# Optimization experiments

Hardware: AMD Instinct MI355X
Metric: run time of the kernel (lower is better)

Reference implementation:

```python
import jax, jax.numpy as jnp
import numpy as np

BN_EPS = 1e-5

def _l2norm(x, axis):
    # F.normalize: x / max(||x||_2, 1e-12)
    n = jnp.sqrt(jnp.sum(x * x, axis=axis, keepdims=True))
    return x / jnp.maximum(n, 1e-12)

def _psi(x_bhc, w, g, b):
    # 1x1 conv over HW-as-channels: [B,HW,C] x [D,HW] -> [B,D,C]
    y = jnp.einsum('dh,bhc->bdc', w, x_bhc)
    # inference BatchNorm2d with running_mean=0, running_var=1
    scale = g / jnp.sqrt(1.0 + BN_EPS)
    y = y * scale[None, :, None] + b[None, :, None]
    return jax.nn.relu(y)

def setup_inputs() -> dict:
    key = jax.random.key(0)
    ks = jax.random.split(key, 8)
    B, C, H, W, D = 16, 2048, 32, 32, 256
    return {
        'v2l_conv_feature': jax.random.normal(ks[0], (B, C, H, W), jnp.float32),
        'l2v_conv_feature': jax.random.normal(ks[1], (B, C, H, W), jnp.float32),
        'w_v2l': jax.random.normal(ks[2], (D, H * W), jnp.float32) * 0.02,
        'g_v2l': jax.random.uniform(ks[3], (D,), jnp.float32, 0.5, 1.5),
        'b_v2l': jax.random.normal(ks[4], (D,), jnp.float32) * 0.1,
        'w_l2v': jax.random.normal(ks[5], (D, H * W), jnp.float32) * 0.02,
        'g_l2v': jax.random.uniform(ks[6], (D,), jnp.float32, 0.5, 1.5),
        'b_l2v': jax.random.normal(ks[7], (D,), jnp.float32) * 0.1,
    }

def reference(v2l_conv_feature, l2v_conv_feature, w_v2l, g_v2l, b_v2l, w_l2v, g_l2v, b_l2v):
    B, C, H, W = v2l_conv_feature.shape
    HW = H * W
    xv = jnp.transpose(v2l_conv_feature.reshape(B, C, HW), (0, 2, 1))  # [B,HW,C]
    xl = jnp.transpose(l2v_conv_feature.reshape(B, C, HW), (0, 2, 1))  # [B,HW,C]
    v2l_adj = _l2norm(_psi(xv, w_v2l, g_v2l, b_v2l), axis=2)  # [B,D,C], norm over C
    l2v_adj = _l2norm(_psi(xl, w_l2v, g_l2v, b_l2v), axis=1)  # [B,D,C], norm over D
    # Faithful to torch: reshape of the permuted tensor is a raw row-major
    # reinterpretation [B,HW,C] -> [B,C,HW] (NOT a transpose back).
    xv_r = xv.reshape(B, C, HW)
    latent = jnp.einsum('bdc,bch->bdh', v2l_adj, xv_r)          # [B,D,HW]
    latent_n = _l2norm(latent, axis=-1)
    aff = jax.nn.softmax(jnp.einsum('bdh,beh->bde', latent_n, latent_n), axis=-1)  # [B,D,D]
    latent = jnp.einsum('bde,beh->bdh', aff, latent)            # [B,D,HW]
    visible = jnp.einsum('bdc,bdh->bch', l2v_adj, latent)       # [B,C,HW]
    return visible.reshape(B, C, H, W)
```

## Files before the change

kernel.cpp:

```cpp
#include <hip/hip_runtime.h>
#include <hip/hip_bf16.h>

#define BB 16
#define CC 2048
#define HWW 1024
#define DD 256
#define BN_RSQRT 0.9999950000374997f

typedef short bf16x8 __attribute__((ext_vector_type(8)));
typedef float f32x4 __attribute__((ext_vector_type(4)));
typedef unsigned short u16x8 __attribute__((ext_vector_type(8)));
typedef unsigned short u16x4 __attribute__((ext_vector_type(4)));
typedef unsigned short u16;

typedef __attribute__((address_space(1))) const unsigned GU;
typedef __attribute__((address_space(3))) unsigned LU;
__device__ __forceinline__ void gload16(const void* g, void* l) {
    __builtin_amdgcn_global_load_lds((GU*)g, (LU*)l, 16, 0, 0);
}

__device__ __forceinline__ unsigned short f2bf(float x) {
    unsigned u = __builtin_bit_cast(unsigned, x);
    unsigned r = u + 0x7FFFu + ((u >> 16) & 1u);
    return (unsigned short)(r >> 16);
}
__device__ __forceinline__ float bf2f(unsigned short h) {
    unsigned u = ((unsigned)h) << 16;
    return __builtin_bit_cast(float, u);
}
__device__ __forceinline__ void split2(float x, unsigned short& hi, unsigned short& lo) {
    hi = f2bf(x);
    lo = f2bf(x - bf2f(hi));
}
__device__ __forceinline__ void split2t(float x, unsigned short& hi, unsigned short& lo) {
    hi = f2bf(x);
    float d = x - bf2f(hi);
    lo = (unsigned short)(__builtin_bit_cast(unsigned, d) >> 16);
}

struct RegsA { u16x8 h[2]; u16x8 l[2]; };
struct RegsB { u16x8 h[2]; u16x8 l[2]; };

__global__ __launch_bounds__(256) void split_k(const float* __restrict__ in,
                                               u16* __restrict__ hi, u16* __restrict__ lo,
                                               long long n8) {
    long long i = (long long)blockIdx.x * 256 + threadIdx.x;
    if (i >= n8) return;
    const float4* p = (const float4*)in + i * 2;
    float4 a = p[0], b = p[1];
    float xs[8] = {a.x, a.y, a.z, a.w, b.x, b.y, b.z, b.w};
    u16x8 h, l;
    #pragma unroll
    for (int j = 0; j < 8; ++j) { unsigned short hh, ll; split2(xs[j], hh, ll); h[j] = hh; l[j] = ll; }
    *(u16x8*)(hi + i * 8) = h;
    *(u16x8*)(lo + i * 8) = l;
}

template <int BF, int EPI, int FUSE2, int KS>
__global__ __launch_bounds__(512, 4) void gemm2b(
    const u16* __restrict__ Ah0, const u16* __restrict__ Al0,
    const u16* __restrict__ Ah1, const u16* __restrict__ Al1,
    long long aB, int lda,
    const void* __restrict__ B0a, const void* __restrict__ B0b,
    const void* __restrict__ B1a, const void* __restrict__ B1b,
    long long bB, int ldb,
    float* __restrict__ C0, float* __restrict__ C1,
    long long cB, long long kB, int ldc,
    int K,
    const float* __restrict__ g0, const float* __restrict__ bb0,
    const float* __restrict__ g1, const float* __restrict__ bb1)
{
    __shared__ __attribute__((aligned(16))) char smem[2][32768];

    const int gx = gridDim.x, gy = gridDim.y;
    int nwg = gx * gy * gridDim.z;
    int id = blockIdx.x + gx * (blockIdx.y + gy * blockIdx.z);
    int chunk = nwg >> 3;
    int nid = (id & 7) * chunk + (id >> 3);
    int bx = nid % gx;
    int tmp = nid / gx;
    int by = tmp % gy;
    int bz = tmp / gy;

    const int t = threadIdx.x;
    const int n0 = bx * 128, m0 = by * 128;

    int op = 0, batch, kz = 0;
    if constexpr (FUSE2) { op = bz >> 4; batch = bz & 15; }
    else if constexpr (KS > 1) { batch = bz / KS; kz = bz - batch * KS; }
    else { batch = bz; }
    const int koffA = kz * K;

    const u16* Ahp = (op ? Ah1 : Ah0) + (long long)batch * aB + koffA;
    const u16* Alp = (op ? Al1 : Al0) + (long long)batch * aB + koffA;
    const float* Bf = nullptr;
    const u16* Bh = nullptr;
    const u16* Bl = nullptr;
    if constexpr (BF == 0) {
        Bf = (const float*)(op ? B1a : B0a) + (long long)batch * bB;
        Bf += ((long long)(koffA >> 10)) * 1024 * ldb + (koffA & 1023);
    } else {
        Bh = (const u16*)(op ? B1a : B0a) + (long long)batch * bB;
        Bl = (const u16*)(op ? B1b : B0b) + (long long)batch * bB;
    }
    float* Cb = ((EPI == 1 && FUSE2) ? (op ? C1 : C0) : C0)
              + (long long)batch * cB + (long long)kz * kB;
    const float* gp = op ? g1 : g0;
    const float* bp = op ? bb1 : bb0;

    const int arow = t >> 2;
    const int aslt = (t & 3) ^ ((t >> 3) & 3);
    const int brow = t >> 3;
    const int bslt = (t & 7) ^ ((t >> 3) & 7);

    const int l = t & 63, w = t >> 6;
    const int wr = w >> 2, wc = w & 3;
    const int rl = l & 15, kq = l >> 4;
    const int fsw = (kq ^ ((rl >> 1) & 3)) * 16;

    f32x4 acc[4][2];
    #pragma unroll
    for (int i = 0; i < 4; ++i)
        #pragma unroll
        for (int j = 0; j < 2; ++j)
            acc[i][j] = (f32x4){0.f, 0.f, 0.f, 0.f};

    auto gstage = [&](int k0, char* sn) {
        const u16* pa = Ahp + (long long)(m0 + arow) * lda + k0 + aslt * 8;
        gload16(pa, sn + t * 16);
        const u16* pl = Alp + (long long)(m0 + arow) * lda + k0 + aslt * 8;
        gload16(pl, sn + 8192 + t * 16);
        if constexpr (BF == 0) {
            const float* pb = Bf + (long long)(n0 + brow) * ldb + k0 + bslt * 4;
            gload16(pb,                       sn + 16384 + t * 16);
            gload16(pb + (long long)64 * ldb, sn + 24576 + t * 16);
        } else {
            const u16* pbh = Bh + (long long)(n0 + arow) * ldb + k0 + aslt * 8;
            gload16(pbh, sn + 16384 + t * 16);
            const u16* pbl = Bl + (long long)(n0 + arow) * ldb + k0 + aslt * 8;
            gload16(pbl, sn + 24576 + t * 16);
        }
    };

    auto readA = [&](const char* sb, bf16x8* fah, bf16x8* fal) {
        #pragma unroll
        for (int i2 = 0; i2 < 4; ++i2) {
            int off = (wr * 64 + i2 * 16 + rl) * 64 + fsw;
            fah[i2] = *(const bf16x8*)(sb + off);
            fal[i2] = *(const bf16x8*)(sb + 8192 + off);
        }
    };
    auto readB = [&](const char* sb, bf16x8* fbh, bf16x8* fbl) {
        #pragma unroll
        for (int j = 0; j < 2; ++j) {
            int row = wc * 32 + j * 16 + rl;
            if constexpr (BF == 0) {
                const char* p = sb + 16384 + row * 128;
                int g = rl & 7;
                float4 x0 = *(const float4*)(p + ((2 * kq) ^ g) * 16);
                float4 x1 = *(const float4*)(p + ((2 * kq + 1) ^ g) * 16);
                float xs[8] = {x0.x, x0.y, x0.z, x0.w, x1.x, x1.y, x1.z, x1.w};
                u16x8 h, lo;
                #pragma unroll
                for (int e = 0; e < 8; ++e) {
                    unsigned short hh, ll; split2t(xs[e], hh, ll);
                    h[e] = hh; lo[e] = ll;
                }
                fbh[j] = __builtin_bit_cast(bf16x8, h);
                fbl[j] = __builtin_bit_cast(bf16x8, lo);
            } else {
                int off = row * 64 + fsw;
                fbh[j] = *(const bf16x8*)(sb + 16384 + off);
                fbl[j] = *(const bf16x8*)(sb + 24576 + off);
            }
        }
    };

    const int NIT = K >> 5;

    gstage(0, smem[0]);
    asm volatile("s_waitcnt vmcnt(0)" ::: "memory");
    __builtin_amdgcn_s_barrier();

    for (int it = 0; it < NIT; ++it) {
        char* sb = smem[it & 1];
        char* sn = smem[(it + 1) & 1];
        const bool more = (it + 1) < NIT;
        if (more) gstage((it + 1) << 5, sn);

        bf16x8 fah[4], fal[4], fbh[2], fbl[2];
        readB(sb, fbh, fbl);
        readA(sb, fah, fal);

        __builtin_amdgcn_s_setprio(1);
        #pragma unroll
        for (int i2 = 0; i2 < 4; ++i2)
            #pragma unroll
            for (int j = 0; j < 2; ++j)
                acc[i2][j] = __builtin_amdgcn_mfma_f32_16x16x32_bf16(fal[i2], fbh[j], acc[i2][j], 0, 0, 0);
        #pragma unroll
        for (int i2 = 0; i2 < 4; ++i2)
            #pragma unroll
            for (int j = 0; j < 2; ++j)
                acc[i2][j] = __builtin_amdgcn_mfma_f32_16x16x32_bf16(fah[i2], fbl[j], acc[i2][j], 0, 0, 0);
        #pragma unroll
        for (int i2 = 0; i2 < 4; ++i2)
            #pragma unroll
            for (int j = 0; j < 2; ++j)
                acc[i2][j] = __builtin_amdgcn_mfma_f32_16x16x32_bf16(fah[i2], fbh[j], acc[i2][j], 0, 0, 0);
        __builtin_amdgcn_s_setprio(0);

        if (more) { asm volatile("s_waitcnt vmcnt(0)" ::: "memory"); }
        __builtin_amdgcn_s_barrier();
    }

    #pragma unroll
    for (int i = 0; i < 4; ++i) {
        #pragma unroll
        for (int r = 0; r < 4; ++r) {
            int row = m0 + wr * 64 + i * 16 + kq * 4 + r;
            float sc = 1.0f, bi = 0.0f;
            if (EPI == 1) { sc = gp[row] * BN_RSQRT; bi = bp[row]; }
            #pragma unroll
            for (int j = 0; j < 2; ++j) {
                int col = n0 + wc * 32 + j * 16 + rl;
                float v = acc[i][j][r];
                if (EPI == 1) v = fmaxf(fmaf(v, sc, bi), 0.0f);
                Cb[(long long)row * ldc + col] = v;
            }
        }
    }
}

template <int BN_, int EPI>
__global__ __launch_bounds__(256) void mfma_gemm(
    const void* __restrict__ Ap, const void* __restrict__ Ap2, long long aB, int lda,
    const void* __restrict__ Bp, const void* __restrict__ Bp2, long long bB, int ldb,
    void* __restrict__ Cp, void* __restrict__ Cp2,
    long long cB, int ldc, int K)
{
    constexpr int NJ   = BN_ / 32;
    constexpr int BNB  = BN_ * 64;
    constexpr int BUFB = 16384 + BN_ * 128;
    __shared__ __attribute__((aligned(16))) char smem[2][BUFB];

    const int gx = gridDim.x, gy = gridDim.y;
    int nwg = gx * gy * gridDim.z;
    int id = blockIdx.x + gx * (blockIdx.y + gy * blockIdx.z);
    int chunk = nwg >> 3;
    int nid = (id & 7) * chunk + (id >> 3);
    int bx = nid % gx;
    int tmp = nid / gx;
    int by = tmp % gy;
    int bz = tmp / gy;

    const int t  = threadIdx.x;
    const int n0 = bx * BN_;
    const int m0 = by * 128;

    const int ar = t >> 1, ag = t & 1;
    const int af = (ar >> 1) & 3;
    const int as0 = (2 * ag) ^ af, as1 = (2 * ag + 1) ^ af;
    const bool bact = (BN_ == 128) || (t < 2 * BN_);
    const int br = (t >> 1) & (BN_ - 1), bg = t & 1;
    const int bf = (br >> 1) & 3;
    const int bs0 = (2 * bg) ^ bf, bs1 = (2 * bg + 1) ^ bf;

    const int l  = t & 63, w = t >> 6;
    const int wr = w >> 1, wc = w & 1;
    const int rl = l & 15, kq = l >> 4;
    const int sw = kq ^ ((rl >> 1) & 3);
    const int aoff = (wr * 64 + rl) * 64 + sw * 16;
    const int boff = (wc * (BN_ / 2) + rl) * 64 + sw * 16;

    const u16* Ahp = (const u16*)Ap  + (long long)bz * aB;
    const u16* Alp = (const u16*)Ap2 + (long long)bz * aB;
    const u16* Bhp = (const u16*)Bp  + (long long)bz * bB;
    const u16* Blp = (const u16*)Bp2 + (long long)bz * bB;

    auto loadA = [&](int k0, RegsA& ra) {
        const u16* ph = Ahp + (long long)(m0 + ar) * lda + k0 + ag * 16;
        const u16* pl = Alp + (long long)(m0 + ar) * lda + k0 + ag * 16;
        ra.h[0] = *(const u16x8*)(ph);
        ra.h[1] = *(const u16x8*)(ph + 8);
        ra.l[0] = *(const u16x8*)(pl);
        ra.l[1] = *(const u16x8*)(pl + 8);
    };
    auto loadB = [&](int k0, RegsB& rb) {
        if (!bact) return;
        const u16* ph = Bhp + (long long)(n0 + br) * ldb + k0 + bg * 16;
        const u16* pl = Blp + (long long)(n0 + br) * ldb + k0 + bg * 16;
        rb.h[0] = *(const u16x8*)(ph);
        rb.h[1] = *(const u16x8*)(ph + 8);
        rb.l[0] = *(const u16x8*)(pl);
        rb.l[1] = *(const u16x8*)(pl + 8);
    };
    auto stageWrite = [&](char* sb, RegsA& ra, RegsB& rb) {
        *(u16x8*)(sb + ar * 64 + as0 * 16) = ra.h[0];
        *(u16x8*)(sb + ar * 64 + as1 * 16) = ra.h[1];
        *(u16x8*)(sb + 8192 + ar * 64 + as0 * 16) = ra.l[0];
        *(u16x8*)(sb + 8192 + ar * 64 + as1 * 16) = ra.l[1];
        if (bact) {
            char* sB = sb + 16384;
            *(u16x8*)(sB + br * 64 + bs0 * 16) = rb.h[0];
            *(u16x8*)(sB + br * 64 + bs1 * 16) = rb.h[1];
            *(u16x8*)(sB + BNB + br * 64 + bs0 * 16) = rb.l[0];
            *(u16x8*)(sB + BNB + br * 64 + bs1 * 16) = rb.l[1];
        }
    };

    f32x4 acc[4][NJ];
    #pragma unroll
    for (int i = 0; i < 4; ++i)
        #pragma unroll
        for (int j = 0; j < NJ; ++j)
            acc[i][j] = (f32x4){0.f, 0.f, 0.f, 0.f};

    RegsA a0, a1;
    RegsB b0, b1;
    const int NIT = K >> 5;

    loadA(0, a0); loadB(0, b0);
    stageWrite(smem[0], a0, b0);
    loadA(32, a1); loadB(32, b1);
    asm volatile("s_waitcnt lgkmcnt(0)" ::: "memory");
    __builtin_amdgcn_s_barrier();

    auto step = [&](int it, char* sb, char* sn, RegsA& pa, RegsB& pb,
                    RegsA& qa, RegsB& qb) {
        bf16x8 fah[4], fal[4], fbh[NJ], fbl[NJ];
        #pragma unroll
        for (int i = 0; i < 4; ++i) {
            fah[i] = *(const bf16x8*)(sb + aoff + i * 1024);
            fal[i] = *(const bf16x8*)(sb + 8192 + aoff + i * 1024);
        }
        #pragma unroll
        for (int j = 0; j < NJ; ++j) {
            fbh[j] = *(const bf16x8*)(sb + 16384 + boff + j * 1024);
            fbl[j] = *(const bf16x8*)(sb + 16384 + BNB + boff + j * 1024);
        }
        if (it + 1 < NIT) stageWrite(sn, pa, pb);
        if (it + 2 < NIT) { loadA((it + 2) << 5, qa); loadB((it + 2) << 5, qb); }
        #pragma unroll
        for (int i = 0; i < 4; ++i)
            #pragma unroll
            for (int j = 0; j < NJ; ++j) {
                acc[i][j] = __builtin_amdgcn_mfma_f32_16x16x32_bf16(fal[i], fbh[j], acc[i][j], 0, 0, 0);
                acc[i][j] = __builtin_amdgcn_mfma_f32_16x16x32_bf16(fah[i], fbl[j], acc[i][j], 0, 0, 0);
                acc[i][j] = __builtin_amdgcn_mfma_f32_16x16x32_bf16(fah[i], fbh[j], acc[i][j], 0, 0, 0);
            }
        asm volatile("s_waitcnt lgkmcnt(0)" ::: "memory");
        __builtin_amdgcn_s_barrier();
    };

    for (int it = 0; it < NIT; it += 2) {
        step(it,     smem[0], smem[1], a1, b1, a0, b0);
        step(it + 1, smem[1], smem[0], a0, b0, a1, b1);
    }

    #pragma unroll
    for (int i = 0; i < 4; ++i) {
        #pragma unroll
        for (int r = 0; r < 4; ++r) {
            int row = m0 + wr * 64 + i * 16 + kq * 4 + r;
            #pragma unroll
            for (int j = 0; j < NJ; ++j) {
                int col = n0 + wc * (BN_ / 2) + j * 16 + rl;
                float v = acc[i][j][r];
                if constexpr (EPI == 0) {
                    ((float*)Cp + (long long)bz * cB)[(long long)row * ldc + col] = v;
                } else {
                    unsigned short hh, ll; split2(v, hh, ll);
                    ((u16*)Cp  + (long long)bz * cB)[(long long)row * ldc + col] = hh;
                    ((u16*)Cp2 + (long long)bz * cB)[(long long)row * ldc + col] = ll;
                }
            }
        }
    }
}

__global__ __launch_bounds__(256) void rownorm_split_perm_k(float* __restrict__ Y) {
    int d = blockIdx.x, b = blockIdx.y, t = threadIdx.x;
    float* row = Y + ((long long)b * DD + d) * CC;
    float4 v0 = ((const float4*)row)[2 * t];
    float4 v1 = ((const float4*)row)[2 * t + 1];
    float s = v0.x * v0.x + v0.y * v0.y + v0.z * v0.z + v0.w * v0.w
            + v1.x * v1.x + v1.y * v1.y + v1.z * v1.z + v1.w * v1.w;
    for (int off = 32; off > 0; off >>= 1) s += __shfl_down(s, off, 64);
    __shared__ float wsum[4];
    __shared__ float ivs;
    int lane = t & 63, w = t >> 6;
    if (lane == 0) wsum[w] = s;
    __syncthreads();
    if (t == 0) ivs = 1.0f / fmaxf(sqrtf(wsum[0] + wsum[1] + wsum[2] + wsum[3]), 1e-12f);
    __syncthreads();
    float iv = ivs;
    float xs[8] = {v0.x * iv, v0.y * iv, v0.z * iv, v0.w * iv,
                   v1.x * iv, v1.y * iv, v1.z * iv, v1.w * iv};
    u16x4 he, ho, le, lo4;
    #pragma unroll
    for (int j = 0; j < 4; ++j) {
        unsigned short hh, ll;
        split2(xs[2 * j], hh, ll);       he[j] = hh; le[j] = ll;
        split2(xs[2 * j + 1], hh, ll);   ho[j] = hh; lo4[j] = ll;
    }
    u16* hi = (u16*)row;
    *(u16x4*)(hi + 4 * t) = he;
    *(u16x4*)(hi + 1024 + 4 * t) = ho;
    *(u16x4*)(hi + 2048 + 4 * t) = le;
    *(u16x4*)(hi + 3072 + 4 * t) = lo4;
}

__global__ __launch_bounds__(256) void colnorm_k(const float* __restrict__ Yl,
                                                 float* __restrict__ rsc) {
    int b = blockIdx.y;
    int c = blockIdx.x * 256 + threadIdx.x;
    const float* base = Yl + (long long)b * DD * CC + c;
    float s = 0.0f;
    for (int d = 0; d < DD; ++d) { float v = base[(long long)d * CC]; s += v * v; }
    rsc[(long long)b * CC + c] = 1.0f / fmaxf(sqrtf(s), 1e-12f);
}

__global__ __launch_bounds__(256) void trans_split_k(const float* __restrict__ in,
                                                     const float* __restrict__ scale,
                                                     u16* __restrict__ hi, u16* __restrict__ lo) {
    __shared__ float tile[32][33];
    int s0 = blockIdx.x * 32, r0 = blockIdx.y * 32, b = blockIdx.z;
    const float* inb = in + (long long)b * DD * CC;
    int tx = threadIdx.x & 31, ty = threadIdx.x >> 5;
    for (int i = ty; i < 32; i += 8)
        tile[i][tx] = inb[(long long)(r0 + i) * CC + s0 + tx];
    __syncthreads();
    for (int i = ty; i < 32; i += 8) {
        float v = tile[tx][i] * scale[(long long)b * CC + s0 + i];
        unsigned short hh, ll; split2(v, hh, ll);
        long long o = (long long)b * DD * CC + (long long)(s0 + i) * DD + r0 + tx;
        hi[o] = hh; lo[o] = ll;
    }
}

__global__ __launch_bounds__(256) void latreduce_k(const float* __restrict__ parts,
                                                   u16* __restrict__ hi, u16* __restrict__ lo,
                                                   u16* __restrict__ thi, u16* __restrict__ tlo) {
    __shared__ float tile[32][33];
    int h0 = blockIdx.x * 32, d0 = blockIdx.y * 32, b = blockIdx.z;
    const long long sL = (long long)DD * HWW;
    const long long ps = (long long)BB * sL;
    const float* base = parts + (long long)b * sL;
    int tx = threadIdx.x & 31, ty = threadIdx.x >> 5;
    for (int i = ty; i < 32; i += 8) {
        long long o = (long long)(d0 + i) * HWW + h0 + tx;
        float s = base[o] + base[o + ps];
        tile[i][tx] = s;
        unsigned short hh, ll; split2(s, hh, ll);
        long long od = (long long)b * sL + o;
        hi[od] = hh; lo[od] = ll;
    }
    __syncthreads();
    for (int i = ty; i < 32; i += 8) {
        float v = tile[tx][i];
        unsigned short hh, ll; split2(v, hh, ll);
        long long ot = (long long)b * sL + (long long)(h0 + i) * DD + d0 + tx;
        thi[ot] = hh; tlo[ot] = ll;
    }
}

__global__ __launch_bounds__(256) void latnorm_k(const float* __restrict__ G,
                                                 float* __restrict__ rs) {
    int i = blockIdx.x * 256 + threadIdx.x;
    int b = i >> 8, d = i & 255;
    float v = G[((long long)b * DD + d) * DD + d];
    rs[i] = 1.0f / fmaxf(sqrtf(v), 1e-12f);
}

__global__ __launch_bounds__(256) void softmax_k(const float* __restrict__ G,
                                                 const float* __restrict__ rs,
                                                 u16* __restrict__ affHi,
                                                 u16* __restrict__ affLo) {
    int d = blockIdx.x, b = blockIdx.y;
    const float* row = G + ((long long)b * DD + d) * DD;
    const float* rsb = rs + (long long)b * DD;
    int t = threadIdx.x;
    float lg = row[t] * rsb[d] * rsb[t];

    float m = lg;
    for (int off = 32; off > 0; off >>= 1) m = fmaxf(m, __shfl_down(m, off, 64));
    __shared__ float wsm[4];
    __shared__ float bm, bs;
    int lane = t & 63, w = t >> 6;
    if (lane == 0) wsm[w] = m;
    __syncthreads();
    if (t == 0) bm = fmaxf(fmaxf(wsm[0], wsm[1]), fmaxf(wsm[2], wsm[3]));
    __syncthreads();
    float e = expf(lg - bm);
    float s = e;
    for (int off = 32; off > 0; off >>= 1) s += __shfl_down(s, off, 64);
    if (lane == 0) wsm[w] = s;
    __syncthreads();
    if (t == 0) bs = wsm[0] + wsm[1] + wsm[2] + wsm[3];
    __syncthreads();
    float v = e / bs;
    unsigned short hh, ll; split2(v, hh, ll);
    long long o = ((long long)b * DD + d) * DD + t;
    affHi[o] = hh; affLo[o] = ll;
}

extern "C" void kernel_launch(void* const* d_in, const int* in_sizes, int n_in,
                              void* d_out, int out_size, void* d_ws, size_t ws_size,
                              hipStream_t stream) {
    const float* v2l   = (const float*)d_in[0];
    const float* l2v   = (const float*)d_in[1];
    const float* w_v2l = (const float*)d_in[2];
    const float* g_v2l = (const float*)d_in[3];
    const float* b_v2l = (const float*)d_in[4];
    const float* w_l2v = (const float*)d_in[5];
    const float* g_l2v = (const float*)d_in[6];
    const float* b_l2v = (const float*)d_in[7];
    float* out = (float*)d_out;

    char* W = (char*)d_ws;
    float* Yv     = (float*)(W + 0);
    float* Yl     = (float*)(W + 33554432);
    u16*   YltHi  = (u16*)(W + 67108864);
    u16*   YltLo  = (u16*)(W + 83886080);
    u16*   latHi  = (u16*)(W + 100663296);
    u16*   latLo  = (u16*)(W + 109051904);
    u16*   latTHi = (u16*)(W + 117440512);
    u16*   latTLo = (u16*)(W + 125829120);
    u16*   l2tHi  = (u16*)(W + 134217728);
    u16*   l2tLo  = (u16*)(W + 142606336);
    float* gram   = (float*)(W + 150994944);
    float* rs     = (float*)(W + 155189248);
    float* rsc    = (float*)(W + 155205632);
    u16*   affHi  = (u16*)(W + 155336704);
    u16*   affLo  = (u16*)(W + 157433856);
    u16*   WvHi   = (u16*)(W + 159531008);
    u16*   WvLo   = WvHi + 262144;
    u16*   WlHi   = WvLo + 262144;
    u16*   WlLo   = WlHi + 262144;

    float* latPart = (float*)d_out;

    const long long sY   = (long long)DD * CC;
    const long long sL   = (long long)DD * HWW;
    const long long sG   = (long long)DD * DD;
    const long long sX   = (long long)CC * HWW;
    const long long sYp  = (long long)DD * 4096;

    split_k<<<128, 256, 0, stream>>>(w_v2l, WvHi, WvLo, 32768);
    split_k<<<128, 256, 0, stream>>>(w_l2v, WlHi, WlLo, 32768);

    gemm2b<0, 1, 1, 1><<<dim3(CC / 128, DD / 128, 32), 512, 0, stream>>>(
        WvHi, WvLo, WlHi, WlLo, 0, HWW,
        v2l, nullptr, l2v, nullptr, sX, HWW,
        Yv, Yl, sY, 0, CC, HWW,
        g_v2l, b_v2l, g_l2v, b_l2v);

    rownorm_split_perm_k<<<dim3(DD, BB), 256, 0, stream>>>(Yv);
    colnorm_k<<<dim3(CC / 256, BB), 256, 0, stream>>>(Yl, rsc);
    trans_split_k<<<dim3(CC / 32, DD / 32, BB), 256, 0, stream>>>(Yl, rsc, YltHi, YltLo);

    gemm2b<0, 0, 0, 2><<<dim3(HWW / 128, DD / 128, 32), 512, 0, stream>>>(
        (const u16*)Yv, (const u16*)Yv + 2048, nullptr, nullptr, sYp, 4096,
        v2l, nullptr, nullptr, nullptr, sX, HWW,
        latPart, nullptr, sL, (long long)BB * sL, HWW, 1024,
        nullptr, nullptr, nullptr, nullptr);

    latreduce_k<<<dim3(HWW / 32, DD / 32, BB), 256, 0, stream>>>(
        latPart, latHi, latLo, latTHi, latTLo);

    mfma_gemm<64, 0><<<dim3(4, 2, BB), 256, 0, stream>>>(
        latHi, latLo, sL, HWW, latHi, latLo, sL, HWW,
        gram, nullptr, sG, DD, HWW);

    latnorm_k<<<dim3(BB * DD / 256), 256, 0, stream>>>(gram, rs);
    softmax_k<<<dim3(DD, BB), 256, 0, stream>>>(gram, rs, affHi, affLo);

    mfma_gemm<128, 2><<<dim3(2, 8, BB), 256, 0, stream>>>(
        latTHi, latTLo, sL, DD, affHi, affLo, sG, DD,
        l2tHi, l2tLo, sL, DD, DD);

    gemm2b<1, 0, 0, 1><<<dim3(HWW / 128, CC / 128, BB), 512, 0, stream>>>(
        YltHi, YltLo, nullptr, nullptr, sY, DD,
        l2tHi, l2tLo, nullptr, nullptr, sL, DD,
        out, nullptr, sX, 0, HWW, DD,
        nullptr, nullptr, nullptr, nullptr);
}
```

Measured before the change: 364.8 us.

## Split fp32 B tiles once into LDS via registers; fuse column norm with transpose

In the GEMM path that reads fp32 B, B is now loaded into registers, split into bf16 hi/lo once per thread, and written to LDS in the same swizzled bf16 layout used by the pre-split path. This replaces re-splitting every fp32 element in each consuming wave's fragment read, and it uses exact rounding for the lo part. Separately, the column-norm and transpose-split kernels are merged into one kernel that stages a 256x32 tile in shared memory, computes the norms there and writes the transposed hi/lo output. This removes a kernel launch and a second read of Yl, at the cost of a large shared tile, extra lgkmcnt waits and register-path global loads.

```diff
diff --git a/kernel.cpp b/kernel.cpp
--- a/kernel.cpp
+++ b/kernel.cpp
@@ -31,11 +31,6 @@
 __device__ __forceinline__ void split2(float x, unsigned short& hi, unsigned short& lo) {
     hi = f2bf(x);
     lo = f2bf(x - bf2f(hi));
-}
-__device__ __forceinline__ void split2t(float x, unsigned short& hi, unsigned short& lo) {
-    hi = f2bf(x);
-    float d = x - bf2f(hi);
-    lo = (unsigned short)(__builtin_bit_cast(unsigned, d) >> 16);
 }
 
 struct RegsA { u16x8 h[2]; u16x8 l[2]; };
@@ -110,8 +105,7 @@
 
     const int arow = t >> 2;
     const int aslt = (t & 3) ^ ((t >> 3) & 3);
-    const int brow = t >> 3;
-    const int bslt = (t & 7) ^ ((t >> 3) & 7);
+    const int bswz = (t & 3) ^ ((arow >> 1) & 3);
 
     const int l = t & 63, w = t >> 6;
     const int wr = w >> 2, wc = w & 3;
@@ -125,22 +119,41 @@
         for (int j = 0; j < 2; ++j)
             acc[i][j] = (f32x4){0.f, 0.f, 0.f, 0.f};
 
+    float4 rb0, rb1;
+
+    auto loadBregs = [&](int k0) {
+        if constexpr (BF == 0) {
+            const float* p = Bf + (long long)(n0 + arow) * ldb + k0 + (t & 3) * 8;
+            rb0 = *(const float4*)p;
+            rb1 = *(const float4*)(p + 4);
+        }
+    };
     auto gstage = [&](int k0, char* sn) {
         const u16* pa = Ahp + (long long)(m0 + arow) * lda + k0 + aslt * 8;
         gload16(pa, sn + t * 16);
         const u16* pl = Alp + (long long)(m0 + arow) * lda + k0 + aslt * 8;
         gload16(pl, sn + 8192 + t * 16);
-        if constexpr (BF == 0) {
-            const float* pb = Bf + (long long)(n0 + brow) * ldb + k0 + bslt * 4;
-            gload16(pb,                       sn + 16384 + t * 16);
-            gload16(pb + (long long)64 * ldb, sn + 24576 + t * 16);
-        } else {
+        if constexpr (BF == 1) {
             const u16* pbh = Bh + (long long)(n0 + arow) * ldb + k0 + aslt * 8;
             gload16(pbh, sn + 16384 + t * 16);
             const u16* pbl = Bl + (long long)(n0 + arow) * ldb + k0 + aslt * 8;
             gload16(pbl, sn + 24576 + t * 16);
         }
     };
+    auto splitWriteB = [&](char* sn) {
+        if constexpr (BF == 0) {
+            float xs[8] = {rb0.x, rb0.y, rb0.z, rb0.w, rb1.x, rb1.y, rb1.z, rb1.w};
+            u16x8 h, lo;
+            #pragma unroll
+            for (int e = 0; e < 8; ++e) {
+                unsigned short hh, ll; split2(xs[e], hh, ll);
+                h[e] = hh; lo[e] = ll;
+            }
+            char* base = sn + 16384 + arow * 64 + bswz * 16;
+            *(u16x8*)(base) = h;
+            *(u16x8*)(base + 8192) = lo;
+        }
+    };
 
     auto readA = [&](const char* sb, bf16x8* fah, bf16x8* fal) {
         #pragma unroll
@@ -153,44 +166,38 @@
     auto readB = [&](const char* sb, bf16x8* fbh, bf16x8* fbl) {
         #pragma unroll
         for (int j = 0; j < 2; ++j) {
-            int row = wc * 32 + j * 16 + rl;
-            if constexpr (BF == 0) {
-                const char* p = sb + 16384 + row * 128;
-                int g = rl & 7;
-                float4 x0 = *(const float4*)(p + ((2 * kq) ^ g) * 16);
-                float4 x1 = *(const float4*)(p + ((2 * kq + 1) ^ g) * 16);
-                float xs[8] = {x0.x, x0.y, x0.z, x0.w, x1.x, x1.y, x1.z, x1.w};
-                u16x8 h, lo;
-                #pragma unroll
-                for (int e = 0; e < 8; ++e) {
-                    unsigned short hh, ll; split2t(xs[e], hh, ll);
-                    h[e] = hh; lo[e] = ll;
-                }
-                fbh[j] = __builtin_bit_cast(bf16x8, h);
-                fbl[j] = __builtin_bit_cast(bf16x8, lo);
-            } else {
-                int off = row * 64 + fsw;
-                fbh[j] = *(const bf16x8*)(sb + 16384 + off);
-                fbl[j] = *(const bf16x8*)(sb + 24576 + off);
-            }
+            int off = (wc * 32 + j * 16 + rl) * 64 + fsw;
+            fbh[j] = *(const bf16x8*)(sb + 16384 + off);
+            fbl[j] = *(const bf16x8*)(sb + 24576 + off);
         }
     };
 
     const int NIT = K >> 5;
 
+    loadBregs(0);
     gstage(0, smem[0]);
+    if constexpr (BF == 0) {
+        asm volatile("s_waitcnt vmcnt(2)" ::: "memory");
+        splitWriteB(smem[0]);
+    }
     asm volatile("s_waitcnt vmcnt(0)" ::: "memory");
+    asm volatile("s_waitcnt lgkmcnt(0)" ::: "memory");
     __builtin_amdgcn_s_barrier();
 
     for (int it = 0; it < NIT; ++it) {
         char* sb = smem[it & 1];
         char* sn = smem[(it + 1) & 1];
         const bool more = (it + 1) < NIT;
-        if (more) gstage((it + 1) << 5, sn);
+        if (more) { loadBregs((it + 1) << 5); gstage((it + 1) << 5, sn); }
 
         bf16x8 fah[4], fal[4], fbh[2], fbl[2];
         readB(sb, fbh, fbl);
         readA(sb, fah, fal);
+
+        if (more && BF == 0) {
+            asm volatile("s_waitcnt vmcnt(2)" ::: "memory");
+            splitWriteB(sn);
+        }
 
         __builtin_amdgcn_s_setprio(1);
         #pragma unroll
@@ -211,6 +218,7 @@
         __builtin_amdgcn_s_setprio(0);
 
         if (more) { asm volatile("s_waitcnt vmcnt(0)" ::: "memory"); }
+        asm volatile("s_waitcnt lgkmcnt(0)" ::: "memory");
         __builtin_amdgcn_s_barrier();
     }
 
@@ -411,30 +419,38 @@
     *(u16x4*)(hi + 3072 + 4 * t) = lo4;
 }
 
-__global__ __launch_bounds__(256) void colnorm_k(const float* __restrict__ Yl,
-                                                 float* __restrict__ rsc) {
-    int b = blockIdx.y;
-    int c = blockIdx.x * 256 + threadIdx.x;
-    const float* base = Yl + (long long)b * DD * CC + c;
+__global__ __launch_bounds__(256) void transnorm_k(const float* __restrict__ Yl,
+                                                   u16* __restrict__ hi, u16* __restrict__ lo) {
+    __shared__ float tile[256][33];
+    __shared__ float part[8][33];
+    __shared__ float invn[32];
+    int c0 = blockIdx.x * 32, b = blockIdx.y;
+    int t = threadIdx.x;
+    int tx = t & 31, ty = t >> 5;
+    const float* base = Yl + (long long)b * DD * CC + c0;
+    for (int d = ty; d < 256; d += 8)
+        tile[d][tx] = base[(long long)d * CC + tx];
+    __syncthreads();
     float s = 0.0f;
-    for (int d = 0; d < DD; ++d) { float v = base[(long long)d * CC]; s += v * v; }
-    rsc[(long long)b * CC + c] = 1.0f / fmaxf(sqrtf(s), 1e-12f);
-}
-
-__global__ __launch_bounds__(256) void trans_split_k(const float* __restrict__ in,
-                                                     const float* __restrict__ scale,
-                                                     u16* __restrict__ hi, u16* __restrict__ lo) {
-    __shared__ float tile[32][33];
-    int s0 = blockIdx.x * 32, r0 = blockIdx.y * 32, b = blockIdx.z;
-    const float* inb = in + (long long)b * DD * CC;
-    int tx = threadIdx.x & 31, ty = threadIdx.x >> 5;
-    for (int i = ty; i < 32; i += 8)
-        tile[i][tx] = inb[(long long)(r0 + i) * CC + s0 + tx];
-    __syncthreads();
-    for (int i = ty; i < 32; i += 8) {
-        float v = tile[tx][i] * scale[(long long)b * CC + s0 + i];
+    #pragma unroll
+    for (int dd = 0; dd < 32; ++dd) {
+        float v = tile[ty * 32 + dd][tx];
+        s += v * v;
+    }
+    part[ty][tx] = s;
+    __syncthreads();
+    if (ty == 0) {
+        float tot = part[0][tx] + part[1][tx] + part[2][tx] + part[3][tx]
+                  + part[4][tx] + part[5][tx] + part[6][tx] + part[7][tx];
+        invn[tx] = 1.0f / fmaxf(sqrtf(tot), 1e-12f);
+    }
+    __syncthreads();
+    long long ob = (long long)b * DD * CC;
+    #pragma unroll 4
+    for (int i = 0; i < 32; ++i) {
+        float v = tile[t][i] * invn[i];
         unsigned short hh, ll; split2(v, hh, ll);
-        long long o = (long long)b * DD * CC + (long long)(s0 + i) * DD + r0 + tx;
+        long long o = ob + (long long)(c0 + i) * DD + t;
         hi[o] = hh; lo[o] = ll;
     }
 }
@@ -531,7 +547,6 @@
     u16*   l2tLo  = (u16*)(W + 142606336);
     float* gram   = (float*)(W + 150994944);
     float* rs     = (float*)(W + 155189248);
-    float* rsc    = (float*)(W + 155205632);
     u16*   affHi  = (u16*)(W + 155336704);
     u16*   affLo  = (u16*)(W + 157433856);
     u16*   WvHi   = (u16*)(W + 159531008);
@@ -557,8 +572,7 @@
         g_v2l, b_v2l, g_l2v, b_l2v);
 
     rownorm_split_perm_k<<<dim3(DD, BB), 256, 0, stream>>>(Yv);
-    colnorm_k<<<dim3(CC / 256, BB), 256, 0, stream>>>(Yl, rsc);
-    trans_split_k<<<dim3(CC / 32, DD / 32, BB), 256, 0, stream>>>(Yl, rsc, YltHi, YltLo);
+    transnorm_k<<<dim3(CC / 32, BB), 256, 0, stream>>>(Yl, YltHi, YltLo);
 
     gemm2b<0, 0, 0, 2><<<dim3(HWW / 128, DD / 128, 32), 512, 0, stream>>>(
         (const u16*)Yv, (const u16*)Yv + 2048, nullptr, nullptr, sYp, 4096,
```

Measured after the change: 345.7 us. 5.3% less time.
